# Kernel optimization log

Hardware: AMD Instinct MI355X
Metric: run time of the kernel (lower is better)

Reference implementation:

```python
import jax, jax.numpy as jnp
import numpy as np
from jax import lax

WD, H, B, SQ, SS, CL = 300, 100, 128, 48, 48, 16
VOCAB, CVOCAB, CD, K = 91557, 53, 16, 3


def setup_inputs() -> dict:
    key = jax.random.key(0)
    ks = jax.random.split(key, 40)
    p = lambda i, shape: jax.random.normal(ks[i], shape, jnp.float32) * 0.02
    inp = {
        'q_words': jax.random.randint(ks[0], (B, SQ), 0, VOCAB),
        'q_chars': jax.random.randint(ks[1], (B, SQ, CL), 0, CVOCAB),
        's_words': jax.random.randint(ks[2], (B, SS), 0, VOCAB),
        's_chars': jax.random.randint(ks[3], (B, SS, CL), 0, CVOCAB),
        'word_emb': p(4, (VOCAB, WD)),
        'char_emb': p(5, (CVOCAB, CD)),
        'conv_w': p(6, (CD, 1, K)),
        'conv_b': p(7, (CD,)),
    }
    din = WD + CD
    for k in range(5):
        d = din + 2 * H * k  # dense connectivity: input grows by 2H per layer
        inp[f'wih{k+1}'] = p(8 + 4 * k, (4 * H, d))
        inp[f'whh{k+1}'] = p(9 + 4 * k, (4 * H, H))
        inp[f'bih{k+1}'] = p(10 + 4 * k, (4 * H,))
        inp[f'bhh{k+1}'] = p(11 + 4 * k, (4 * H,))
    inp['fcl_w'] = p(30, (800, 5 * H))
    inp['fcl_b'] = p(31, (800,))
    inp['last_w'] = p(32, (2, 800))
    inp['last_b'] = p(33, (2,))
    return inp


def _lstm_scan(x, wih, whh, bih, bhh):
    # x: [S, B, D] -> hidden states [S, B, H]; zero initial state (PyTorch LSTMCell default)
    h0 = jnp.zeros((x.shape[1], H), x.dtype)
    def step(carry, xt):
        h, c = carry
        g = xt @ wih.T + bih + h @ whh.T + bhh
        i, f, gg, o = jnp.split(g, 4, axis=-1)
        c = jax.nn.sigmoid(f) * c + jax.nn.sigmoid(i) * jnp.tanh(gg)
        h = jax.nn.sigmoid(o) * jnp.tanh(c)
        return (h, c), h
    _, hs = lax.scan(step, (h0, h0), x)
    return hs


def _embed(words, chars, word_emb, char_emb, conv_w, conv_b):
    w_e = word_emb[words]  # [B, S, WD]
    Bn, S, Cl = chars.shape
    ce = char_emb[chars].reshape(Bn * S, 1, Cl * CD)  # flatten chars per token
    raw = lax.conv_general_dilated(ce, conv_w, (1,), 'VALID',
                                   dimension_numbers=('NCH', 'OIH', 'NCH'))
    raw = (raw + conv_b[None, :, None]).reshape(Bn, S, CD, -1)
    pooled = jnp.max(jax.nn.relu(raw), axis=-1)        # [B, S, CD]
    pooled0 = jnp.max(raw[0], axis=-1)                 # original quirk: batch row 0 has no relu
    char_e = pooled.at[0].set(pooled0)
    return jnp.concatenate([w_e, char_e], axis=2).transpose(1, 0, 2)  # [S, B, WD+CD]


def _forward(q_words, q_chars, s_words, s_chars, word_emb, char_emb, conv_w, conv_b,
             cells, fcl_w, fcl_b, last_w, last_b):
    px = _embed(q_words, q_chars, word_emb, char_emb, conv_w, conv_b)
    hx = _embed(s_words, s_chars, word_emb, char_emb, conv_w, conv_b)
    hps = hhs = None
    for (wih, whh, bih, bhh) in cells:
        p_h = _lstm_scan(px, wih, whh, bih, bhh)  # [Sp, B, H]
        h_h = _lstm_scan(hx, wih, whh, bih, bhh)  # [Sh, B, H]
        hps = p_h.transpose(1, 0, 2)              # [B, Sp, H]
        hhs = h_h.transpose(1, 0, 2)              # [B, Sh, H]
        attn = jnp.einsum('bph,bqh->bpq', hps, hhs)
        a_p = jnp.einsum('bpq,bqh->bph', jax.nn.softmax(attn, axis=2), hhs)
        a_h = jnp.einsum('bqp,bph->bqh', jax.nn.softmax(attn.transpose(0, 2, 1), axis=2), hps)
        px = jnp.concatenate([px, a_p.transpose(1, 0, 2), p_h], axis=2)
        hx = jnp.concatenate([hx, a_h.transpose(1, 0, 2), h_h], axis=2)
    hq = jnp.max(hps, axis=1)  # max-pool over time
    hs = jnp.max(hhs, axis=1)
    feats = jnp.concatenate([hq, hs, hs - hq, hq * hs, jnp.abs(hq - hs)], axis=1)
    out = jax.nn.relu(feats @ fcl_w.T + fcl_b) @ last_w.T + last_b
    return jax.nn.sigmoid(out)


def reference(q_words, q_chars, s_words, s_chars, word_emb, char_emb, conv_w, conv_b,
              wih1, whh1, bih1, bhh1, wih2, whh2, bih2, bhh2, wih3, whh3, bih3, bhh3,
              wih4, whh4, bih4, bhh4, wih5, whh5, bih5, bhh5,
              fcl_w, fcl_b, last_w, last_b):
    cells = [(wih1, whh1, bih1, bhh1), (wih2, whh2, bih2, bhh2), (wih3, whh3, bih3, bhh3),
             (wih4, whh4, bih4, bhh4), (wih5, whh5, bih5, bhh5)]
    return _forward(q_words, q_chars, s_words, s_chars, word_emb, char_emb, conv_w, conv_b,
                    cells, fcl_w, fcl_b, last_w, last_b)
```

## Files before the change

### kernel.cpp

```cpp
#include <hip/hip_runtime.h>

typedef unsigned short u16;
typedef unsigned int   u32;

#define B_   128
#define S_   48
#define H_   100
#define G_   400
#define PXP  1120

__device__ __forceinline__ float b2f(u16 u) {
    union { u32 i; float f; } v; v.i = ((u32)u) << 16; return v.f;
}
__device__ __forceinline__ u16 f2b(float f) {
    union { float f; u32 i; } v; v.f = f;
    u32 r = v.i + 0x7FFF + ((v.i >> 16) & 1);
    return (u16)(r >> 16);
}

__device__ __forceinline__ float fsig(float x) { return 1.f / (1.f + __expf(-x)); }
__device__ __forceinline__ float ftanh(float x) {
    const float t = __expf(-2.f * fabsf(x));
    const float r = (1.f - t) / (1.f + t);
    return copysignf(r, x);
}

__device__ __forceinline__ float rl(float v0, float v1, int u) {
    return __int_as_float(
        u < 64 ? __builtin_amdgcn_readlane(__float_as_int(v0), u)
               : __builtin_amdgcn_readlane(__float_as_int(v1), u - 64));
}

__device__ __forceinline__ float ldw(const void* p, long i, int bf) {
    return bf ? b2f(((const u16*)p)[i]) : ((const float*)p)[i];
}

__global__ __launch_bounds__(256) void detect_kernel(const void* wemb, int* flag)
{
    const int t = threadIdx.x;
    __shared__ int s;
    if (t == 0) s = 0;
    __syncthreads();
    int bad = 0;
    const u16* p = (const u16*)wemb;
    for (int i = t; i < 4096; i += 256) {
        float v = b2f(p[i]);
        if (!(fabsf(v) < 1e4f)) bad = 1;
    }
    if (bad) atomicOr(&s, 1);
    __syncthreads();
    if (t == 0) *flag = s ? 0 : 1;
}

__global__ __launch_bounds__(64) void embed_kernel(
    const int* __restrict__ qw, const int* __restrict__ qc,
    const int* __restrict__ sw, const int* __restrict__ sc,
    const void* __restrict__ wemb, const void* __restrict__ cemb,
    const void* __restrict__ cw, const void* __restrict__ cb,
    u16* __restrict__ px, u16* __restrict__ hx, const int* __restrict__ flagp)
{
    const int bf = *flagp;
    const int b = blockIdx.x, s = blockIdx.y, seq = blockIdx.z;
    const int* words = seq ? sw : qw;
    const int* chars = seq ? sc : qc;
    u16* dst = seq ? hx : px;
    const int t = threadIdx.x;

    u16* row = dst + (long)(s * B_ + b) * PXP;
    const int w = words[b * S_ + s];
    if (bf) {
        const u32* src = (const u32*)((const u16*)wemb + (long)w * 300);
        u32* d32 = (u32*)row;
        for (int d = t; d < 150; d += 64) d32[d] = src[d];
    } else {
        const float* src = (const float*)wemb + (long)w * 300;
        for (int d = t; d < 300; d += 64) row[d] = f2b(src[d]);
    }

    __shared__ float ce[256];
    const int* ch = chars + (b * S_ + s) * 16;
    for (int j = t; j < 256; j += 64) {
        int ci = ch[j >> 4];
        ce[j] = ldw(cemb, ci * 16 + (j & 15), bf);
    }
    __syncthreads();

    float cwr[3][16], cbr[16];
#pragma unroll
    for (int oc = 0; oc < 16; ++oc) {
        cbr[oc] = ldw(cb, oc, bf);
#pragma unroll
        for (int kk = 0; kk < 3; ++kk) cwr[kk][oc] = ldw(cw, oc * 3 + kk, bf);
    }

    float vmax[16];
#pragma unroll
    for (int oc = 0; oc < 16; ++oc) vmax[oc] = -1e30f;

    for (int p = t; p < 254; p += 64) {
        float c0 = ce[p], c1 = ce[p + 1], c2 = ce[p + 2];
#pragma unroll
        for (int oc = 0; oc < 16; ++oc) {
            float v = fmaf(c0, cwr[0][oc], fmaf(c1, cwr[1][oc], fmaf(c2, cwr[2][oc], cbr[oc])));
            vmax[oc] = fmaxf(vmax[oc], v);
        }
    }
#pragma unroll
    for (int m = 32; m; m >>= 1) {
#pragma unroll
        for (int oc = 0; oc < 16; ++oc)
            vmax[oc] = fmaxf(vmax[oc], __shfl_xor(vmax[oc], m));
    }
    if (t == 0) {
#pragma unroll
        for (int oc = 0; oc < 16; ++oc) {
            float v = vmax[oc];
            if (b != 0) v = fmaxf(v, 0.f);
            row[300 + oc] = f2b(v);
        }
    }
}

#if defined(__gfx950__)

typedef __attribute__((ext_vector_type(4))) float f32x4;
typedef __attribute__((ext_vector_type(8))) __bf16 bf16x8;
#define LDPB 72
#define BK   64

__device__ __forceinline__ void gload_lds16(const void* g, void* l) {
    __builtin_amdgcn_global_load_lds(
        (const __attribute__((address_space(1))) u32*)g,
        (__attribute__((address_space(3))) u32*)l, 16, 0, 0);
}

__global__ __launch_bounds__(256) void gemm_wih(
    const u16* __restrict__ px, const u16* __restrict__ hx,
    float* __restrict__ Xg_p, float* __restrict__ Xg_h,
    const void* __restrict__ wih, const void* __restrict__ bih,
    const void* __restrict__ bhh, int K, const int* __restrict__ flagp)
{
    const int bf = *flagp;
    const u16* A = blockIdx.z ? hx : px;
    float* C = blockIdx.z ? Xg_h : Xg_p;
    const int m0 = blockIdx.x * 128, n0 = blockIdx.y * 64;

    __shared__ __align__(16) u16 As0[128 * 64];
    __shared__ __align__(16) u16 As1[128 * 64];
    __shared__ __align__(16) u16 Bs0[64 * LDPB];
    __shared__ __align__(16) u16 Bs1[64 * LDPB];

    const int tid  = threadIdx.x;
    const int lane = tid & 63;
    const int w    = tid >> 6;
    const int fr   = lane & 15;
    const int fq   = lane >> 4;

    const int rb = tid >> 2;
    const int kb = (tid & 3) * 16;
    const int nB = n0 + rb;
    const int bok = nB < G_;

    const int arow = lane >> 3;
    const int achk = (lane & 7) ^ arow;
    const u16* aLane = A + (long)(m0 + w * 32 + arow) * PXP + achk * 8;

    const u16* wp = (const u16*)wih;
    const u16* bSrc = wp + (long)nB * K + kb;

    f32x4 acc[2][4] = {};

    auto loadB = [&](int k0, uint2* br4) {
        if (bok) {
            const u16* bp = bSrc + k0;
#pragma unroll
            for (int i = 0; i < 4; ++i) br4[i] = *(const uint2*)(bp + i * 4);
        } else {
#pragma unroll
            for (int i = 0; i < 4; ++i) { br4[i].x = 0u; br4[i].y = 0u; }
        }
    };
    auto stageA = [&](u16* dstAs, int k0) {
#pragma unroll
        for (int c = 0; c < 4; ++c)
            gload_lds16(aLane + (long)c * 8 * PXP + k0,
                        &dstAs[(w * 32 + c * 8) * 64]);
    };
    auto writeB = [&](u16* dstBs, const uint2* br4) {
        u16* bs = &dstBs[rb * LDPB + kb];
#pragma unroll
        for (int i = 0; i < 4; ++i) *(uint2*)(bs + i * 4) = br4[i];
    };
    auto compute = [&](const u16* As_, const u16* Bs_) {
#pragma unroll
        for (int ks = 0; ks < BK; ks += 32) {
            const int sw = (((ks >> 3) + fq) ^ (fr & 7)) * 8;
            bf16x8 a0 = *(const bf16x8*)&As_[(w * 32 + fr) * 64 + sw];
            bf16x8 a1 = *(const bf16x8*)&As_[(w * 32 + 16 + fr) * 64 + sw];
#pragma unroll
            for (int j = 0; j < 4; ++j) {
                bf16x8 bj = *(const bf16x8*)&Bs_[(j * 16 + fr) * LDPB + ks + fq * 8];
                acc[0][j] = __builtin_amdgcn_mfma_f32_16x16x32_bf16(a0, bj, acc[0][j], 0, 0, 0);
                acc[1][j] = __builtin_amdgcn_mfma_f32_16x16x32_bf16(a1, bj, acc[1][j], 0, 0, 0);
            }
        }
    };

    const int nfull = K / BK;

    {
        uint2 br4[4];
        loadB(0, br4);
        stageA(As0, 0);
        writeB(Bs0, br4);
    }
    asm volatile("s_waitcnt vmcnt(0) lgkmcnt(0)" ::: "memory");
    __builtin_amdgcn_s_barrier();

    int t = 0;
    while (t < nfull) {
        if (t + 1 < nfull) {
            uint2 br4[4];
            loadB((t + 1) * BK, br4);
            stageA(As1, (t + 1) * BK);
            writeB(Bs1, br4);
        }
        compute(As0, Bs0);
        asm volatile("s_waitcnt vmcnt(0) lgkmcnt(0)" ::: "memory");
        __builtin_amdgcn_s_barrier();
        ++t;
        if (t >= nfull) break;

        if (t + 1 < nfull) {
            uint2 br4[4];
            loadB((t + 1) * BK, br4);
            stageA(As0, (t + 1) * BK);
            writeB(Bs0, br4);
        }
        compute(As1, Bs1);
        asm volatile("s_waitcnt vmcnt(0) lgkmcnt(0)" ::: "memory");
        __builtin_amdgcn_s_barrier();
        ++t;
    }

    const int k0 = nfull * BK;
    if (k0 < K) {
        {
            const int ra = tid >> 1;
            const int ka = (tid & 1) * 32;
            const u16* ar = A + (long)(m0 + ra) * PXP;
            const u16* br = wp + (long)nB * K;
            u16* bs = &Bs0[rb * LDPB + kb];
#pragma unroll
            for (int c = 0; c < 4; ++c) {
                const int o0 = ka + c * 8;
                u16* dst = &As0[ra * 64 + (((o0 >> 3) ^ (ra & 7)) * 8)];
                if (k0 + o0 + 8 <= K) {
                    *(float4*)dst = *(const float4*)(ar + k0 + o0);
                } else {
#pragma unroll
                    for (int i = 0; i < 8; ++i) {
                        const int k = k0 + o0 + i;
                        dst[i] = (k < K) ? ar[k] : (u16)0;
                    }
                }
            }
#pragma unroll
            for (int c = 0; c < 4; ++c) {
                const int o0 = kb + c * 4;
                if (bok && k0 + o0 + 4 <= K) {
                    *(uint2*)(bs + o0 - kb) = *(const uint2*)(br + k0 + o0);
                } else {
#pragma unroll
                    for (int i = 0; i < 4; ++i) {
                        const int k = k0 + o0 + i;
                        bs[o0 - kb + i] = (bok && k < K) ? br[k] : (u16)0;
                    }
                }
            }
        }
        __syncthreads();
        const int ksend = ((K - k0 + 31) & ~31);
        for (int ks = 0; ks < ksend; ks += 32) {
            const int sw = (((ks >> 3) + fq) ^ (fr & 7)) * 8;
            bf16x8 a0 = *(const bf16x8*)&As0[(w * 32 + fr) * 64 + sw];
            bf16x8 a1 = *(const bf16x8*)&As0[(w * 32 + 16 + fr) * 64 + sw];
#pragma unroll
            for (int j = 0; j < 4; ++j) {
                bf16x8 bj = *(const bf16x8*)&Bs0[(j * 16 + fr) * LDPB + ks + fq * 8];
                acc[0][j] = __builtin_amdgcn_mfma_f32_16x16x32_bf16(a0, bj, acc[0][j], 0, 0, 0);
                acc[1][j] = __builtin_amdgcn_mfma_f32_16x16x32_bf16(a1, bj, acc[1][j], 0, 0, 0);
            }
        }
    }

#pragma unroll
    for (int j = 0; j < 4; ++j) {
        const int col = n0 + j * 16 + fr;
        if (col < G_) {
            const float bias = ldw(bih, col, bf) + ldw(bhh, col, bf);
#pragma unroll
            for (int m = 0; m < 2; ++m)
#pragma unroll
                for (int i = 0; i < 4; ++i) {
                    const int row = m0 + w * 32 + m * 16 + fq * 4 + i;
                    C[(long)row * G_ + col] = acc[m][j][i] + bias;
                }
        }
    }
}
#undef LDPB
#undef BK

#else

__global__ __launch_bounds__(256) void gemm_wih(
    const u16* __restrict__ px, const u16* __restrict__ hx,
    float* __restrict__ Xg_p, float* __restrict__ Xg_h,
    const void* __restrict__ wih, const void* __restrict__ bih,
    const void* __restrict__ bhh, int K, const int* __restrict__ flagp)
{
    const int bf = *flagp;
    const u16* A = blockIdx.z ? hx : px;
    float* C = blockIdx.z ? Xg_h : Xg_p;

    __shared__ float As[16][64];
    __shared__ float Bs[16][64];

    const int tid = threadIdx.x;
    const int tx = tid & 15, ty = tid >> 4;
    const int m0 = blockIdx.x * 64, n0 = blockIdx.y * 64;
    const int lr = tid >> 2, lk = (tid & 3) * 4;

    float acc[4][4] = {};

    for (int k0 = 0; k0 < K; k0 += 16) {
        const u16* Ap = A + (long)(m0 + lr) * PXP + k0 + lk;
#pragma unroll
        for (int u = 0; u < 4; ++u)
            As[lk + u][lr] = (k0 + lk + u < K) ? b2f(Ap[u]) : 0.f;
        {
            const int n = n0 + lr;
#pragma unroll
            for (int u = 0; u < 4; ++u) {
                const int kk = k0 + lk + u;
                Bs[lk + u][lr] = (n < G_ && kk < K) ? ldw(wih, (long)n * K + kk, bf) : 0.f;
            }
        }
        __syncthreads();
#pragma unroll
        for (int k = 0; k < 16; ++k) {
            float a[4], bq[4];
#pragma unroll
            for (int i = 0; i < 4; ++i) a[i] = As[k][ty * 4 + i];
#pragma unroll
            for (int j = 0; j < 4; ++j) bq[j] = Bs[k][tx * 4 + j];
#pragma unroll
            for (int i = 0; i < 4; ++i)
#pragma unroll
                for (int j = 0; j < 4; ++j)
                    acc[i][j] = fmaf(a[i], bq[j], acc[i][j]);
        }
        __syncthreads();
    }

#pragma unroll
    for (int j = 0; j < 4; ++j) {
        const int col = n0 + tx * 4 + j;
        if (col < G_) {
            const float bias = ldw(bih, col, bf) + ldw(bhh, col, bf);
#pragma unroll
            for (int i = 0; i < 4; ++i)
                C[(long)(m0 + ty * 4 + i) * G_ + col] = acc[i][j] + bias;
        }
    }
}

#endif

__global__ __launch_bounds__(448, 2)
void lstm_scan(
    const float* __restrict__ Xg_p, const float* __restrict__ Xg_h,
    const void* __restrict__ whh,
    float* __restrict__ p_h, float* __restrict__ h_h,
    u16* __restrict__ px, u16* __restrict__ hx, int cat_off,
    const int* __restrict__ flagp)
{
    const int bf = *flagp;
    const int b = blockIdx.x, seq = blockIdx.y;
    const float* Xg = seq ? Xg_h : Xg_p;
    float* hout = seq ? h_h : p_h;
    u16* xcat = seq ? hx : px;
    const int g = threadIdx.x;
    const int l = g & 63;

    __shared__ float h_lds[128];
    __shared__ float g_lds[400];
    __shared__ float h_hist[S_ * 104];

    u32 wpk[50];
    float xg = 0.f;
    if (g < G_) {
        if (bf) {
            const u32* w2 = (const u32*)whh;
#pragma unroll
            for (int j = 0; j < 50; ++j) wpk[j] = w2[g * 50 + j];
        } else {
            const float* wf = (const float*)whh;
#pragma unroll
            for (int j = 0; j < 50; ++j) {
                u32 lo = f2b(wf[(long)g * 100 + 2 * j]);
                u32 hi = f2b(wf[(long)g * 100 + 2 * j + 1]);
                wpk[j] = lo | (hi << 16);
            }
        }
#pragma unroll
        for (int j = 0; j < 50; ++j) asm volatile("" : "+v"(wpk[j]));
        xg = Xg[(long)b * G_ + g];
    }
    if (g < 128) h_lds[g] = 0.f;
    float c_reg = 0.f;
    __syncthreads();

    for (int s = 0; s < S_; ++s) {
        const float hv0 = h_lds[l];
        const float hv1 = h_lds[l + 64];
        if (g < G_) {
            float a0 = xg, a1 = 0.f, a2 = 0.f, a3 = 0.f;
#pragma unroll
            for (int u = 0; u < 100; u += 4) {
                const u32 p0 = wpk[u >> 1], p1 = wpk[(u >> 1) + 1];
                const float w0 = __int_as_float(p0 << 16);
                const float w1 = __int_as_float(p0 & 0xFFFF0000u);
                const float w2 = __int_as_float(p1 << 16);
                const float w3 = __int_as_float(p1 & 0xFFFF0000u);
                a0 = fmaf(rl(hv0, hv1, u),     w0, a0);
                a1 = fmaf(rl(hv0, hv1, u + 1), w1, a1);
                a2 = fmaf(rl(hv0, hv1, u + 2), w2, a2);
                a3 = fmaf(rl(hv0, hv1, u + 3), w3, a3);
            }
            g_lds[g] = (a0 + a1) + (a2 + a3);
            if (s + 1 < S_) xg = Xg[(long)((s + 1) * B_ + b) * G_ + g];
        }
        asm volatile("s_waitcnt lgkmcnt(0)" ::: "memory");
        __builtin_amdgcn_s_barrier();
        if (g < H_) {
            const float iv = fsig(g_lds[g]);
            const float fv = fsig(g_lds[100 + g]);
            const float gv = ftanh(g_lds[200 + g]);
            const float ov = fsig(g_lds[300 + g]);
            c_reg = fv * c_reg + iv * gv;
            const float hv = ov * ftanh(c_reg);
            h_lds[g] = hv;
            h_hist[s * 104 + g] = hv;
        }
        asm volatile("s_waitcnt lgkmcnt(0)" ::: "memory");
        __builtin_amdgcn_s_barrier();
    }

    for (int i = g; i < S_ * H_; i += 448) {
        const int s = i / H_, d = i - s * H_;
        const float hv = h_hist[s * 104 + d];
        hout[(long)(s * B_ + b) * H_ + d] = hv;
        if (cat_off >= 0) xcat[(long)(s * B_ + b) * PXP + cat_off + d] = f2b(hv);
    }
}

__global__ __launch_bounds__(256) void attn_kernel(
    const float* __restrict__ p_h, const float* __restrict__ h_h,
    u16* __restrict__ px, u16* __restrict__ hx, int off)
{
    const int b = blockIdx.x, dir = blockIdx.y, t = threadIdx.x;
    __shared__ __align__(16) float P[4800], Q[4800];
    __shared__ float A[2304], Sx[2304];

    {
        float4* P4 = (float4*)P;
        float4* Q4 = (float4*)Q;
        for (int i = t; i < 1200; i += 256) {
            const int s = i / 25, d4 = i % 25;
            P4[i] = *(const float4*)(p_h + (long)(s * B_ + b) * H_ + d4 * 4);
            Q4[i] = *(const float4*)(h_h + (long)(s * B_ + b) * H_ + d4 * 4);
        }
    }
    __syncthreads();

    for (int e = t; e < 2304; e += 256) {
        const int p = e / 48, q = e % 48;
        const float4* Pr = (const float4*)&P[p * 100];
        const float4* Qr = (const float4*)&Q[q * 100];
        float a0 = 0.f, a1 = 0.f;
#pragma unroll
        for (int j = 0; j < 25; ++j) {
            const float4 u = Pr[j], v = Qr[j];
            a0 = fmaf(u.x, v.x, a0); a1 = fmaf(u.y, v.y, a1);
            a0 = fmaf(u.z, v.z, a0); a1 = fmaf(u.w, v.w, a1);
        }
        A[e] = a0 + a1;
    }
    __syncthreads();

    if (t < 48) {
        if (dir == 0) {
            float m = -1e30f;
            for (int q = 0; q < 48; ++q) m = fmaxf(m, A[t * 48 + q]);
            float sum = 0.f;
            for (int q = 0; q < 48; ++q) {
                const float e = __expf(A[t * 48 + q] - m);
                Sx[t * 48 + q] = e;
                sum += e;
            }
            const float inv = 1.f / sum;
            for (int q = 0; q < 48; ++q) Sx[t * 48 + q] *= inv;
        } else {
            float m = -1e30f;
            for (int p = 0; p < 48; ++p) m = fmaxf(m, A[p * 48 + t]);
            float sum = 0.f;
            for (int p = 0; p < 48; ++p) {
                const float e = __expf(A[p * 48 + t] - m);
                Sx[p * 48 + t] = e;
                sum += e;
            }
            const float inv = 1.f / sum;
            for (int p = 0; p < 48; ++p) Sx[p * 48 + t] *= inv;
        }
    }
    __syncthreads();

    if (dir == 0) {
        for (int e = t; e < 4800; e += 256) {
            const int p = e / 100, d = e % 100;
            float acc = 0.f;
            for (int q = 0; q < 48; ++q) acc = fmaf(Sx[p * 48 + q], Q[q * 100 + d], acc);
            px[(long)(p * B_ + b) * PXP + off + d] = f2b(acc);
        }
    } else {
        for (int e = t; e < 4800; e += 256) {
            const int q = e / 100, d = e % 100;
            float acc = 0.f;
            for (int p = 0; p < 48; ++p) acc = fmaf(Sx[p * 48 + q], P[p * 100 + d], acc);
            hx[(long)(q * B_ + b) * PXP + off + d] = f2b(acc);
        }
    }
}

__global__ __launch_bounds__(256) void pool_feats(
    const float* __restrict__ p_h, const float* __restrict__ h_h,
    float* __restrict__ featsT)
{
    const int t = blockIdx.x * 256 + threadIdx.x;
    if (t >= B_ * H_) return;
    const int b = t / H_, u = t % H_;
    float hq = -1e30f, hs = -1e30f;
    for (int s = 0; s < S_; ++s) {
        hq = fmaxf(hq, p_h[(long)(s * B_ + b) * H_ + u]);
        hs = fmaxf(hs, h_h[(long)(s * B_ + b) * H_ + u]);
    }
    featsT[(      u) * B_ + b] = hq;
    featsT[(100 + u) * B_ + b] = hs;
    featsT[(200 + u) * B_ + b] = hs - hq;
    featsT[(300 + u) * B_ + b] = hq * hs;
    featsT[(400 + u) * B_ + b] = fabsf(hq - hs);
}

__global__ __launch_bounds__(256) void fcl_kernel(
    const float* __restrict__ featsT, const void* __restrict__ fw,
    const void* __restrict__ fb, float* __restrict__ zT, const int* __restrict__ flagp)
{
    const int bf = *flagp;
    const int t = blockIdx.x * 256 + threadIdx.x;
    const int o = t >> 7, b = t & 127;
    float acc = ldw(fb, o, bf);
    const long wrow = (long)o * 500;
    for (int d = 0; d < 500; ++d) acc = fmaf(featsT[d * B_ + b], ldw(fw, wrow + d, bf), acc);
    zT[o * B_ + b] = fmaxf(acc, 0.f);
}

__global__ __launch_bounds__(256) void last_kernel(
    const float* __restrict__ zT, const void* __restrict__ lw,
    const void* __restrict__ lb, void* __restrict__ out, const int* __restrict__ flagp)
{
    const int bf = *flagp;
    const int b = blockIdx.x, t = threadIdx.x;
    const int c = t >> 7;
    const int u = t & 127;
    __shared__ float red[4];

    float part = 0.f;
    for (int o = u; o < 800; o += 128)
        part = fmaf(zT[o * B_ + b], ldw(lw, (long)c * 800 + o, bf), part);
#pragma unroll
    for (int m = 32; m; m >>= 1) part += __shfl_xor(part, m);
    if ((t & 63) == 0) red[t >> 6] = part;
    __syncthreads();
    if (t < 2) {
        const float acc = red[2 * t] + red[2 * t + 1] + ldw(lb, t, bf);
        const float v = 1.f / (1.f + expf(-acc));
        if (bf) ((u16*)out)[b * 2 + t] = f2b(v);
        else    ((float*)out)[b * 2 + t] = v;
    }
}

extern "C" void kernel_launch(void* const* d_in, const int* in_sizes, int n_in,
                              void* d_out, int out_size, void* d_ws, size_t ws_size,
                              hipStream_t stream)
{
    (void)in_sizes; (void)n_in; (void)out_size; (void)ws_size;

    const int* qw = (const int*)d_in[0];
    const int* qc = (const int*)d_in[1];
    const int* sw = (const int*)d_in[2];
    const int* sc = (const int*)d_in[3];
    const void* wemb = d_in[4];
    const void* cemb = d_in[5];
    const void* cw   = d_in[6];
    const void* cb   = d_in[7];
    const void* fclw = d_in[28];
    const void* fclb = d_in[29];
    const void* lw   = d_in[30];
    const void* lb   = d_in[31];

    float* ws = (float*)d_ws;
    int*  flag = (int*)ws;
    u16* px   = (u16*)(ws + 16);
    u16* hx   = px + (long)S_ * B_ * PXP;
    float* Xg_p = (float*)(hx + (long)S_ * B_ * PXP);
    float* Xg_h = Xg_p + (long)S_ * B_ * G_;
    float* p_h  = Xg_h + (long)S_ * B_ * G_;
    float* h_h  = p_h + (long)S_ * B_ * H_;
    float* featsT = h_h + (long)S_ * B_ * H_;
    float* zT   = featsT + 500 * B_;

    detect_kernel<<<dim3(1), 256, 0, stream>>>(wemb, flag);

    embed_kernel<<<dim3(B_, S_, 2), 64, 0, stream>>>(qw, qc, sw, sc, wemb, cemb, cw, cb, px, hx, flag);

    for (int k = 0; k < 5; ++k) {
        const void* wih = d_in[8 + 4 * k];
        const void* whh = d_in[9 + 4 * k];
        const void* bih = d_in[10 + 4 * k];
        const void* bhh = d_in[11 + 4 * k];
        const int K = 316 + 200 * k;

        gemm_wih<<<dim3(48, 7, 2), 256, 0, stream>>>(px, hx, Xg_p, Xg_h, wih, bih, bhh, K, flag);

        const int cat = (k < 4) ? (K + 100) : -1;
        lstm_scan<<<dim3(B_, 2), 448, 0, stream>>>(Xg_p, Xg_h, whh, p_h, h_h, px, hx, cat, flag);

        if (k < 4)
            attn_kernel<<<dim3(B_, 2), 256, 0, stream>>>(p_h, h_h, px, hx, K);
    }

    pool_feats<<<dim3(50), 256, 0, stream>>>(p_h, h_h, featsT);
    fcl_kernel<<<dim3(400), 256, 0, stream>>>(featsT, fclw, fclb, zT, flag);
    last_kernel<<<dim3(B_), 256, 0, stream>>>(zT, lw, lb, d_out, flag);
}
```

Before: 790.9 us.

## Compute LSTM cell update redundantly in every wave to drop second barrier

Each wave now reads all gate pre-activations from a double-buffered gate array in shared memory and computes the cell and hidden update for units l and 64+l itself, so h stays in registers. This removes the hidden-state broadcast through shared memory and the second barrier of each timestep. In exchange every wave does redundant transcendental work for all units (and garbage for units 100-127). The double buffer keeps a fast wave from overwriting gates that a slower wave is still reading.

New measurement: 890.1 us. +12.5%, slower.

```diff
diff --git a/kernel.cpp b/kernel.cpp
--- a/kernel.cpp
+++ b/kernel.cpp
@@ -394,13 +394,14 @@
     const int g = threadIdx.x;
     const int l = g & 63;
 
-    __shared__ float h_lds[128];
-    __shared__ float g_lds[400];
+    __shared__ float g_lds[2][4][128];
     __shared__ float h_hist[S_ * 104];
 
     u32 wpk[50];
     float xg = 0.f;
+    int gate = 0, unit = 0;
     if (g < G_) {
+        gate = g / 100; unit = g - gate * 100;
         if (bf) {
             const u32* w2 = (const u32*)whh;
 #pragma unroll
@@ -418,13 +419,14 @@
         for (int j = 0; j < 50; ++j) asm volatile("" : "+v"(wpk[j]));
         xg = Xg[(long)b * G_ + g];
     }
-    if (g < 128) h_lds[g] = 0.f;
-    float c_reg = 0.f;
+    for (int i = g; i < 2 * 4 * 128; i += 448) ((float*)g_lds)[i] = 0.f;
+
+    float hv0 = 0.f, hv1 = 0.f;
+    float c0 = 0.f, c1 = 0.f;
     __syncthreads();
 
     for (int s = 0; s < S_; ++s) {
-        const float hv0 = h_lds[l];
-        const float hv1 = h_lds[l + 64];
+        const int buf = s & 1;
         if (g < G_) {
             float a0 = xg, a1 = 0.f, a2 = 0.f, a3 = 0.f;
 #pragma unroll
@@ -439,24 +441,31 @@
                 a2 = fmaf(rl(hv0, hv1, u + 2), w2, a2);
                 a3 = fmaf(rl(hv0, hv1, u + 3), w3, a3);
             }
-            g_lds[g] = (a0 + a1) + (a2 + a3);
+            g_lds[buf][gate][unit] = (a0 + a1) + (a2 + a3);
             if (s + 1 < S_) xg = Xg[(long)((s + 1) * B_ + b) * G_ + g];
         }
         asm volatile("s_waitcnt lgkmcnt(0)" ::: "memory");
         __builtin_amdgcn_s_barrier();
-        if (g < H_) {
-            const float iv = fsig(g_lds[g]);
-            const float fv = fsig(g_lds[100 + g]);
-            const float gv = ftanh(g_lds[200 + g]);
-            const float ov = fsig(g_lds[300 + g]);
-            c_reg = fv * c_reg + iv * gv;
-            const float hv = ov * ftanh(c_reg);
-            h_lds[g] = hv;
-            h_hist[s * 104 + g] = hv;
-        }
-        asm volatile("s_waitcnt lgkmcnt(0)" ::: "memory");
-        __builtin_amdgcn_s_barrier();
-    }
+        {
+            const float iv0 = fsig(g_lds[buf][0][l]);
+            const float fv0 = fsig(g_lds[buf][1][l]);
+            const float gv0 = ftanh(g_lds[buf][2][l]);
+            const float ov0 = fsig(g_lds[buf][3][l]);
+            c0 = fv0 * c0 + iv0 * gv0;
+            hv0 = ov0 * ftanh(c0);
+            const float iv1 = fsig(g_lds[buf][0][64 + l]);
+            const float fv1 = fsig(g_lds[buf][1][64 + l]);
+            const float gv1 = ftanh(g_lds[buf][2][64 + l]);
+            const float ov1 = fsig(g_lds[buf][3][64 + l]);
+            c1 = fv1 * c1 + iv1 * gv1;
+            hv1 = ov1 * ftanh(c1);
+            if (g < 64) {
+                h_hist[s * 104 + l] = hv0;
+                if (l < 36) h_hist[s * 104 + 64 + l] = hv1;
+            }
+        }
+    }
+    __syncthreads();
 
     for (int i = g; i < S_ * H_; i += 448) {
         const int s = i / H_, d = i - s * H_;
```
